# Kernel tuning notes

Measured on AMD Instinct MI355X. Metric: run time of the kernel, lower is better.

Reference implementation:

```python
import jax, jax.numpy as jnp
import numpy as np

B, T, C = 4, 2048, 1024
H, Dh = 16, 64
EPS = 1e-5

def _layernorm(x, g, b):
    mu = jnp.mean(x, axis=-1, keepdims=True)
    var = jnp.mean(jnp.square(x - mu), axis=-1, keepdims=True)
    return (x - mu) * jax.lax.rsqrt(var + EPS) * g + b

def setup_inputs() -> dict:
    key = jax.random.key(0)
    ks = jax.random.split(key, 12)
    s = lambda fan_in: 1.0 / np.sqrt(fan_in)
    return {
        "x":  jax.random.normal(ks[0], (B, T, C), dtype=jnp.float32),
        "Wq": jax.random.uniform(ks[1], (C, H * Dh), jnp.float32, -s(C), s(C)),
        "Wk": jax.random.uniform(ks[2], (C, H * Dh), jnp.float32, -s(C), s(C)),
        "Wv": jax.random.uniform(ks[3], (C, H * Dh), jnp.float32, -s(C), s(C)),
        "Wo": jax.random.uniform(ks[4], (H * Dh, C), jnp.float32, -s(H * Dh), s(H * Dh)),
        "bo": jnp.zeros((C,), jnp.float32),
        "W1": jax.random.uniform(ks[5], (C, 4 * C), jnp.float32, -s(C), s(C)),
        "b1": jnp.zeros((4 * C,), jnp.float32),
        "W2": jax.random.uniform(ks[6], (4 * C, C), jnp.float32, -s(4 * C), s(4 * C)),
        "b2": jnp.zeros((C,), jnp.float32),
        "g1": jnp.ones((C,), jnp.float32),
        "be1": jnp.zeros((C,), jnp.float32),
        "g2": jnp.ones((C,), jnp.float32),
        "be2": jnp.zeros((C,), jnp.float32),
    }

def reference(x, Wq, Wk, Wv, Wo, bo, W1, b1, W2, b2, g1, be1, g2, be2):
    # --- pre-LN attention ---
    h = _layernorm(x, g1, be1)                                   # [B,T,C]
    q = (h @ Wq).reshape(B, T, H, Dh)                            # per-head projections fused
    k = (h @ Wk).reshape(B, T, H, Dh)
    v = (h @ Wv).reshape(B, T, H, Dh)
    scores = jnp.einsum('bqhd,bkhd->bhqk', q, k) * (Dh ** -0.5)  # [B,H,T,T]
    causal = jnp.tril(jnp.ones((T, T), dtype=bool))
    scores = jnp.where(causal, scores, -jnp.inf)
    wei = jax.nn.softmax(scores, axis=-1)                        # dropout p=0 (eval)
    attn = jnp.einsum('bhqk,bkhd->bqhd', wei, v).reshape(B, T, H * Dh)
    x = x + attn @ Wo + bo
    # --- pre-LN MLP ---
    h2 = _layernorm(x, g2, be2)
    x = x + jax.nn.relu(h2 @ W1 + b1) @ W2 + b2
    return x
```

## Files before the change

### kernel.cpp

```cpp
#include <hip/hip_runtime.h>
#include <hip/hip_bf16.h>

typedef __hip_bfloat16 bf16;
typedef __attribute__((ext_vector_type(8))) short short8;
typedef __attribute__((ext_vector_type(4))) short s16x4;
typedef __attribute__((ext_vector_type(4))) float f32x4;

__device__ __forceinline__ float s2f(short s) {
    unsigned u = ((unsigned)(unsigned short)s) << 16;
    return __builtin_bit_cast(float, u);
}
__device__ __forceinline__ short f2s(float f) {
    bf16 h = __float2bfloat16(f);
    return __builtin_bit_cast(short, h);
}
__device__ __forceinline__ void gload_lds16(const void* g, void* l) {
    __builtin_amdgcn_global_load_lds(
        (const __attribute__((address_space(1))) unsigned int*)g,
        (__attribute__((address_space(3))) unsigned int*)l, 16, 0, 0);
}

#define PH_VM8  asm volatile("s_waitcnt vmcnt(8)" ::: "memory")
#define PH_VM4  asm volatile("s_waitcnt vmcnt(4)" ::: "memory")
#define PH_VM0  asm volatile("s_waitcnt vmcnt(0)" ::: "memory")
#define PH_BAR  __builtin_amdgcn_s_barrier()
#define PH_LGKM do { asm volatile("s_waitcnt lgkmcnt(0)" ::: "memory"); \
                     __builtin_amdgcn_sched_barrier(0); } while (0)

__global__ __launch_bounds__(256) void tconv_kernel(const float* __restrict__ src,
                                                    short* __restrict__ dst,
                                                    int R, int C) {
    __shared__ short tile[64][65];
    const int r0 = blockIdx.y * 64, c0 = blockIdx.x * 64;
    const int t = threadIdx.x;
    const int lr = t >> 2, lc = (t & 3) * 16;
    const float* sp = src + (size_t)(r0 + lr) * C + c0 + lc;
#pragma unroll
    for (int q = 0; q < 4; q++) {
        f32x4 v = *(const f32x4*)(const void*)(sp + q * 4);
#pragma unroll
        for (int j = 0; j < 4; j++) tile[lr][lc + q * 4 + j] = f2s(v[j]);
    }
    __syncthreads();
    short8 o0, o1;
#pragma unroll
    for (int j = 0; j < 8; j++) { o0[j] = tile[lc + j][lr]; o1[j] = tile[lc + 8 + j][lr]; }
    short* dp = dst + (size_t)(c0 + lr) * R + r0 + lc;
    *(short8*)(void*)dp = o0;
    *(short8*)(void*)(dp + 8) = o1;
}

__global__ __launch_bounds__(256) void ln_kernel(const float* __restrict__ x,
                                                 const float* __restrict__ g,
                                                 const float* __restrict__ beta,
                                                 bf16* __restrict__ out) {
    const int t = threadIdx.x;
    const int w = t >> 6, lane = t & 63;
    const int row = blockIdx.x * 4 + w;
    const float* xr = x + (size_t)row * 1024;
    float v[16];
    float s = 0.f, ss = 0.f;
#pragma unroll
    for (int p = 0; p < 4; p++) {
        f32x4 xv = *(const f32x4*)(const void*)(xr + p * 256 + lane * 4);
#pragma unroll
        for (int j = 0; j < 4; j++) {
            v[p * 4 + j] = xv[j];
            s += xv[j];
            ss += xv[j] * xv[j];
        }
    }
#pragma unroll
    for (int off = 32; off >= 1; off >>= 1) {
        s += __shfl_xor(s, off);
        ss += __shfl_xor(ss, off);
    }
    const float mu = s * (1.0f / 1024.0f);
    const float var = ss * (1.0f / 1024.0f) - mu * mu;
    const float rstd = rsqrtf(var + 1e-5f);
    short* orow = (short*)(void*)(out + (size_t)row * 1024);
#pragma unroll
    for (int p = 0; p < 4; p++) {
        const int c = p * 256 + lane * 4;
        f32x4 gv = *(const f32x4*)(const void*)(g + c);
        f32x4 bv = *(const f32x4*)(const void*)(beta + c);
        s16x4 o;
#pragma unroll
        for (int j = 0; j < 4; j++)
            o[j] = f2s((v[p * 4 + j] - mu) * rstd * gv[j] + bv[j]);
        *(s16x4*)(void*)(orow + c) = o;
    }
}

__global__ __launch_bounds__(256) void gemm64(const bf16* __restrict__ A,
                                              const bf16* __restrict__ Bt,
                                              const float* __restrict__ bias,
                                              const float* resid,
                                              void* Cp, int c_f32,
                                              int m_base, int N, int K,
                                              int relu_flag) {
    __shared__ short As[64 * 64];
    __shared__ short Bs[64 * 64];

    const int t = threadIdx.x;
    const int m0 = blockIdx.x * 64;
    const int n0 = blockIdx.y * 64;
    const int w = t >> 6;
    const int lane = t & 63;
    const int wm = (w >> 1) * 32;
    const int wn = (w & 1) * 32;

    const int sr = t >> 2, sk = (t & 3) * 8;
    const bf16* aA = A + (size_t)(m0 + sr) * K + sk;
    const bf16* aB = Bt + (size_t)(n0 + sr) * K + sk;
    short* ldsA0 = &As[w * 512];
    short* ldsA1 = &As[2048 + w * 512];
    short* ldsB0 = &Bs[w * 512];
    short* ldsB1 = &Bs[2048 + w * 512];

    const int l = lane & 15;
    const int lk = (lane >> 4) * 8;

    f32x4 acc[2][2] = {};

    for (int k0 = 0; k0 < K; k0 += 64) {
        __syncthreads();
        gload_lds16(aA + k0, ldsA0);
        gload_lds16(aA + k0 + 32, ldsA1);
        gload_lds16(aB + k0, ldsB0);
        gload_lds16(aB + k0 + 32, ldsB1);
        __syncthreads();
#pragma unroll
        for (int ks = 0; ks < 2; ks++) {
            short8 a0 = *(const short8*)&As[ks * 2048 + (wm + l) * 32 + lk];
            short8 a1 = *(const short8*)&As[ks * 2048 + (wm + 16 + l) * 32 + lk];
            short8 b0 = *(const short8*)&Bs[ks * 2048 + (wn + l) * 32 + lk];
            short8 b1 = *(const short8*)&Bs[ks * 2048 + (wn + 16 + l) * 32 + lk];
            acc[0][0] = __builtin_amdgcn_mfma_f32_16x16x32_bf16(a0, b0, acc[0][0], 0, 0, 0);
            acc[0][1] = __builtin_amdgcn_mfma_f32_16x16x32_bf16(a0, b1, acc[0][1], 0, 0, 0);
            acc[1][0] = __builtin_amdgcn_mfma_f32_16x16x32_bf16(a1, b0, acc[1][0], 0, 0, 0);
            acc[1][1] = __builtin_amdgcn_mfma_f32_16x16x32_bf16(a1, b1, acc[1][1], 0, 0, 0);
        }
    }

    const int lrow4 = (lane >> 4) * 4;
#pragma unroll
    for (int mi = 0; mi < 2; mi++)
#pragma unroll
        for (int r = 0; r < 4; r++) {
            const int grow = m_base + m0 + wm + mi * 16 + lrow4 + r;
#pragma unroll
            for (int ni = 0; ni < 2; ni++) {
                const int gcol = n0 + wn + ni * 16 + l;
                float val = acc[mi][ni][r];
                if (bias) val += bias[gcol];
                if (relu_flag) val = fmaxf(val, 0.f);
                const size_t ci = (size_t)grow * N + gcol;
                if (resid) val += resid[ci];
                if (c_f32) ((float*)Cp)[ci] = val;
                else        ((short*)Cp)[ci] = f2s(val);
            }
        }
}

#define MM_BLOCK(ACC)                                                        \
    do {                                                                     \
        __builtin_amdgcn_s_setprio(1);                                       \
        _Pragma("unroll")                                                    \
        for (int mi_ = 0; mi_ < 4; mi_++)                                    \
            _Pragma("unroll")                                                \
            for (int ni_ = 0; ni_ < 4; ni_++)                                \
                ACC[mi_][ni_] = __builtin_amdgcn_mfma_f32_16x16x32_bf16(     \
                    af[mi_], bf[ni_], ACC[mi_][ni_], 0, 0, 0);               \
        __builtin_amdgcn_s_setprio(0);                                       \
    } while (0)

__global__ __launch_bounds__(512, 2) void gemm256(const bf16* __restrict__ A,
                                                  const bf16* __restrict__ Bt,
                                                  const float* __restrict__ bias,
                                                  bf16* __restrict__ Cp,
                                                  int N, int relu_flag) {
    __shared__ char lds[131072];
    constexpr int NT = 16;

    const int t = threadIdx.x;
    const int w = t >> 6, lane = t & 63;
    const int l = lane & 15, g = lane >> 4;
    const int m0 = blockIdx.x * 256, n0 = blockIdx.y * 256;
    const int wm = (w >> 2) * 128, wn = (w & 3) * 64;
    const int qx = (g ^ ((l >> 1) & 3)) * 16;
    const int qh8 = (((lane & 3) ^ ((lane >> 3) & 3)) * 8);
    const int srow = w * 32 + (lane >> 2);
    const short* Asrc = (const short*)A;
    const short* Bsrc = (const short*)Bt;

    f32x4 accL[4][4] = {};
    f32x4 accH[4][4] = {};
    short8 af[4], bf[4];

    auto stage = [&](int th, int j) {
        const int ks = j >> 1, mat = j & 1;
        char* slot = lds + ((th & 1) << 16) + (mat << 15) + (ks << 14);
        const short* mp = mat ? Bsrc : Asrc;
        const int rowb = (mat ? n0 : m0);
        const int kc = th * 64 + ks * 32 + qh8;
        gload_lds16(mp + (size_t)(rowb + srow) * 1024 + kc,      slot + (w * 2) * 1024);
        gload_lds16(mp + (size_t)(rowb + srow + 16) * 1024 + kc, slot + (w * 2 + 1) * 1024);
    };
    auto lda = [&](const char* rb, int mi, int ks) -> short8 {
        return *(const short8*)(rb + (ks << 14) + (wm + mi * 16 + l) * 64 + qx);
    };
    auto ldb = [&](const char* rb, int ni, int ks) -> short8 {
        return *(const short8*)(rb + 32768 + (ks << 14) + (wn + ni * 16 + l) * 64 + qx);
    };

    stage(0, 0); stage(0, 1); stage(0, 2); stage(0, 3); stage(1, 0); stage(1, 1);

    for (int it = 0; it < NT - 1; ++it) {
        const char* rb = lds + ((it & 1) << 16);
        PH_VM8; PH_BAR;
#pragma unroll
        for (int i = 0; i < 4; i++) af[i] = lda(rb, i, 0);
#pragma unroll
        for (int i = 0; i < 4; i++) bf[i] = ldb(rb, i, 0);
        stage(it + 1, 2);
        PH_LGKM;
        MM_BLOCK(accL);
#pragma unroll
        for (int i = 0; i < 4; i++) af[i] = lda(rb, 4 + i, 0);
        stage(it + 1, 3);
        PH_BAR; PH_LGKM;
        MM_BLOCK(accH);
        PH_VM8; PH_BAR;
#pragma unroll
        for (int i = 0; i < 4; i++) af[i] = lda(rb, i, 1);
#pragma unroll
        for (int i = 0; i < 4; i++) bf[i] = ldb(rb, i, 1);
        if (it + 2 < NT) stage(it + 2, 0);
        PH_LGKM;
        MM_BLOCK(accL);
#pragma unroll
        for (int i = 0; i < 4; i++) af[i] = lda(rb, 4 + i, 1);
        if (it + 2 < NT) stage(it + 2, 1);
        PH_BAR; PH_LGKM;
        MM_BLOCK(accH);
    }
    {
        const char* rb = lds + (((NT - 1) & 1) << 16);
        PH_VM4; PH_BAR;
#pragma unroll
        for (int i = 0; i < 4; i++) af[i] = lda(rb, i, 0);
#pragma unroll
        for (int i = 0; i < 4; i++) bf[i] = ldb(rb, i, 0);
        PH_LGKM;
        MM_BLOCK(accL);
#pragma unroll
        for (int i = 0; i < 4; i++) af[i] = lda(rb, 4 + i, 0);
        PH_BAR; PH_LGKM;
        MM_BLOCK(accH);
        PH_VM0; PH_BAR;
#pragma unroll
        for (int i = 0; i < 4; i++) af[i] = lda(rb, i, 1);
#pragma unroll
        for (int i = 0; i < 4; i++) bf[i] = ldb(rb, i, 1);
        PH_LGKM;
        MM_BLOCK(accL);
#pragma unroll
        for (int i = 0; i < 4; i++) af[i] = lda(rb, 4 + i, 1);
        PH_BAR; PH_LGKM;
        MM_BLOCK(accH);
    }

#pragma unroll
    for (int half = 0; half < 2; half++)
#pragma unroll
        for (int mi = 0; mi < 4; mi++)
#pragma unroll
            for (int r = 0; r < 4; r++) {
                const int grow = m0 + wm + (half * 4 + mi) * 16 + g * 4 + r;
                short* crow = (short*)(void*)Cp + (size_t)grow * N;
#pragma unroll
                for (int ni = 0; ni < 4; ni++) {
                    const int gcol = n0 + wn + ni * 16 + l;
                    float val = half ? accH[mi][ni][r] : accL[mi][ni][r];
                    if (bias) val += bias[gcol];
                    if (relu_flag) val = fmaxf(val, 0.f);
                    crow[gcol] = f2s(val);
                }
            }
}

__global__ __launch_bounds__(256) void attn_kernel(const bf16* __restrict__ qkv,
                                                   bf16* __restrict__ o) {
    __shared__ short KsF[2][4096];
    __shared__ short Vt[64][72];
    __shared__ short Pl[4][32][76];

    const int bh = blockIdx.x;
    const int b = bh >> 4, h = bh & 15;
    const int qt = 15 - blockIdx.y;
    const int q0 = qt * 128;
    const size_t rbase = (size_t)b * 2048;
    const int hcol = h * 64;

    const int t = threadIdx.x;
    const int w = t >> 6;
    const int lane = t & 63;
    const int l = lane & 15;
    const int g = lane >> 4;
    const int sp = t >> 3;
    const int sb = (t & 7) * 8;

    const int qw0 = q0 + 32 * w;
    short8 qf[2][2];
#pragma unroll
    for (int mi = 0; mi < 2; mi++)
#pragma unroll
        for (int ks = 0; ks < 2; ks++) {
            const short* qp = (const short*)qkv +
                (rbase + qw0 + mi * 16 + l) * 3072 + hcol + ks * 32 + g * 8;
            short8 tv = *(const short8*)(const void*)qp;
            short8 sv;
#pragma unroll
            for (int e = 0; e < 8; e++) sv[e] = f2s(s2f(tv[e]) * 0.125f);
            qf[mi][ks] = sv;
        }

    const int key_a = w * 16 + (lane >> 3);
    const int kd = (lane & 7) ^ ((lane >> 3) & 7);
    const short* kgA = (const short*)qkv + (rbase + key_a) * 3072 + 1024 + hcol + kd * 8;
    const short* kgB = kgA + 8 * 3072;

    f32x4 o_acc[2][4] = {};
    f32x4 l_acc[2] = {};
    short8 onesf;
    {
        const short ov = (l == 0) ? (short)0x3F80 : (short)0;
#pragma unroll
        for (int e = 0; e < 8; e++) onesf[e] = ov;
    }
    const f32x4 s_init = {-12.f, -12.f, -12.f, -12.f};

    const int kt_max = (q0 + 127) >> 6;

    gload_lds16(kgA, &KsF[0][w * 1024]);
    gload_lds16(kgB, &KsF[0][w * 1024 + 512]);

    for (int kt = 0; kt <= kt_max; kt++) {
        const int k0 = kt * 64;
        const short* vg = (const short*)qkv + (rbase + k0 + 2 * sp) * 3072 + 2048 + hcol + sb;
        short8 vv0 = *(const short8*)(const void*)vg;
        short8 vv1 = *(const short8*)(const void*)(vg + 3072);
        PH_BAR;
        {
            const int kp = (kt < kt_max) ? (kt + 1) : kt;
            const size_t kof = (size_t)kp * 64 * 3072;
            gload_lds16(kgA + kof, &KsF[(kt + 1) & 1][w * 1024]);
            gload_lds16(kgB + kof, &KsF[(kt + 1) & 1][w * 1024 + 512]);
        }
        asm volatile("s_waitcnt vmcnt(2)" ::: "memory");
        __builtin_amdgcn_sched_barrier(0);
        {
            const int key = 2 * sp;
            const int cbk = key >> 3;
            const int kin = key & 7;
#pragma unroll
            for (int j = 0; j < 8; j++) {
                const int d = sb + j;
                const int col = ((cbk ^ (d >> 3)) << 3) + kin;
                int pk = (int)(unsigned short)vv0[j] | ((int)(unsigned short)vv1[j] << 16);
                *(int*)(void*)&Vt[d][col] = pk;
            }
        }
        asm volatile("s_waitcnt lgkmcnt(0)" ::: "memory");
        __builtin_amdgcn_sched_barrier(0);
        PH_BAR;

        if (k0 <= qw0 + 31) {
            const short* kb = &KsF[kt & 1][0];
            const bool needMask = (k0 + 63 > qw0);
            f32x4 s_acc[2][4];
#pragma unroll
            for (int mi = 0; mi < 2; mi++)
#pragma unroll
                for (int ni = 0; ni < 4; ni++) s_acc[mi][ni] = s_init;
#pragma unroll
            for (int ks = 0; ks < 2; ks++) {
                short8 kf[4];
#pragma unroll
                for (int ni = 0; ni < 4; ni++) {
                    const int key = ni * 16 + l;
                    const int c = key * 8 + ((ks * 4 + g) ^ (key & 7));
                    kf[ni] = *(const short8*)&kb[c * 8];
                }
#pragma unroll
                for (int mi = 0; mi < 2; mi++)
#pragma unroll
                    for (int ni = 0; ni < 4; ni++)
                        s_acc[mi][ni] = __builtin_amdgcn_mfma_f32_16x16x32_bf16(
                            qf[mi][ks], kf[ni], s_acc[mi][ni], 0, 0, 0);
            }
#pragma unroll
            for (int mi = 0; mi < 2; mi++)
#pragma unroll
                for (int r = 0; r < 4; r++) {
                    const int qg = qw0 + mi * 16 + 4 * g + r;
#pragma unroll
                    for (int ni = 0; ni < 4; ni++) {
                        float s = s_acc[mi][ni][r];
                        if (needMask && (k0 + ni * 16 + l > qg)) s = -1e30f;
                        Pl[w][mi * 16 + 4 * g + r][ni * 16 + l] = f2s(__expf(s));
                    }
                }
#pragma unroll
            for (int ks = 0; ks < 2; ks++) {
                short8 pf[2], vf[4];
#pragma unroll
                for (int mi = 0; mi < 2; mi++)
                    pf[mi] = *(const short8*)&Pl[w][mi * 16 + l][ks * 32 + g * 8];
#pragma unroll
                for (int nd = 0; nd < 4; nd++) {
                    const int d = nd * 16 + l;
                    const int cb = ks * 4 + g;
                    vf[nd] = *(const short8*)&Vt[d][((cb ^ (d >> 3)) << 3)];
                }
#pragma unroll
                for (int mi = 0; mi < 2; mi++) {
                    l_acc[mi] = __builtin_amdgcn_mfma_f32_16x16x32_bf16(
                        pf[mi], onesf, l_acc[mi], 0, 0, 0);
#pragma unroll
                    for (int nd = 0; nd < 4; nd++)
                        o_acc[mi][nd] = __builtin_amdgcn_mfma_f32_16x16x32_bf16(
                            pf[mi], vf[nd], o_acc[mi][nd], 0, 0, 0);
                }
            }
        }
    }

#pragma unroll
    for (int mi = 0; mi < 2; mi++)
#pragma unroll
        for (int r = 0; r < 4; r++) {
            float lsum = __shfl(l_acc[mi][r], lane & 48);
            const float inv = 1.0f / lsum;
            const int qg = qw0 + mi * 16 + 4 * g + r;
            short* op = (short*)(void*)(o + (rbase + qg) * 1024 + hcol);
#pragma unroll
            for (int nd = 0; nd < 4; nd++)
                op[nd * 16 + l] = f2s(o_acc[mi][nd][r] * inv);
        }
}

extern "C" void kernel_launch(void* const* d_in, const int* in_sizes, int n_in,
                              void* d_out, int out_size, void* d_ws, size_t ws_size,
                              hipStream_t stream) {
    const float* x   = (const float*)d_in[0];
    const float* Wq  = (const float*)d_in[1];
    const float* Wk  = (const float*)d_in[2];
    const float* Wv  = (const float*)d_in[3];
    const float* Wo  = (const float*)d_in[4];
    const float* bo  = (const float*)d_in[5];
    const float* W1  = (const float*)d_in[6];
    const float* b1  = (const float*)d_in[7];
    const float* W2  = (const float*)d_in[8];
    const float* b2  = (const float*)d_in[9];
    const float* g1  = (const float*)d_in[10];
    const float* be1 = (const float*)d_in[11];
    const float* g2  = (const float*)d_in[12];
    const float* be2 = (const float*)d_in[13];

    char* ws = (char*)d_ws;
    const size_t MB = (size_t)1024 * 1024;
    bf16*  s0  = (bf16*)(ws);
    bf16*  qkv = (bf16*)(ws + 16 * MB);
    short* WoT = (short*)(ws + 16 * MB);
    short* W1T = (short*)(ws);
    short* W2T = (short*)(ws + 8 * MB);
    bf16*  h2  = (bf16*)(ws + 16 * MB);
    bf16*  m1  = (bf16*)(ws + 32 * MB);
    short* WT  = (short*)d_out;
    float* x1  = (float*)d_out;

    const int M = 8192, C = 1024, F = 4096, MH = 4096;

    tconv_kernel<<<dim3(16, 16), 256, 0, stream>>>(Wq, WT,                   C, C);
    tconv_kernel<<<dim3(16, 16), 256, 0, stream>>>(Wk, WT + 1024 * 1024,     C, C);
    tconv_kernel<<<dim3(16, 16), 256, 0, stream>>>(Wv, WT + 2 * 1024 * 1024, C, C);

    ln_kernel<<<M / 4, 256, 0, stream>>>(x, g1, be1, s0);

    gemm256<<<dim3(M / 256, 3072 / 256), 512, 0, stream>>>(
        s0, (const bf16*)WT, nullptr, qkv, 3072, 0);

    attn_kernel<<<dim3(64, 16), 256, 0, stream>>>(qkv, s0);

    tconv_kernel<<<dim3(16, 16), 256, 0, stream>>>(Wo, WoT, C, C);
    gemm64<<<dim3(M / 64, C / 64), 256, 0, stream>>>(
        s0, (const bf16*)WoT, bo, x, x1, 1, 0, C, C, 0);

    tconv_kernel<<<dim3(64, 16), 256, 0, stream>>>(W1, W1T, C, F);
    tconv_kernel<<<dim3(16, 64), 256, 0, stream>>>(W2, W2T, F, C);

    ln_kernel<<<M / 4, 256, 0, stream>>>(x1, g2, be2, h2);

    for (int half = 0; half < 2; half++) {
        const bf16* Ah = h2 + (size_t)half * MH * C;
        gemm256<<<dim3(MH / 256, F / 256), 512, 0, stream>>>(
            Ah, (const bf16*)W1T, b1, m1, F, 1);
        gemm64<<<dim3(MH / 64, C / 64), 256, 0, stream>>>(
            m1, (const bf16*)W2T, b2, x1, d_out, 1, half * MH, C, F, 0);
    }
}
```

Baseline: 562.0 us.

## Transpose score MFMA for vectorized P stores, compute row sums in registers; swizzle GEMM blocks

The attention kernel swaps the MFMA operands so each lane holds four consecutive keys of one query row. The P tile can then be written to LDS with one 4-element vector store instead of scalar stores. The softmax denominator becomes a per-lane register sum finished with cross-lane shuffles, which removes the extra ones-vector MFMA per step. Separately, the GEMM remaps block indices with an 8-way swizzle to change the order tiles are scheduled, probably for L2 or cross-chip cache locality. This adds a few shuffles and index arithmetic, and the P store layout now depends on the transposed accumulator mapping.

```diff
diff --git a/kernel.cpp b/kernel.cpp
--- a/kernel.cpp
+++ b/kernel.cpp
@@ -186,7 +186,13 @@
     const int t = threadIdx.x;
     const int w = t >> 6, lane = t & 63;
     const int l = lane & 15, g = lane >> 4;
-    const int m0 = blockIdx.x * 256, n0 = blockIdx.y * 256;
+
+    const int nwg = gridDim.x * gridDim.y;
+    const int orig = blockIdx.y * gridDim.x + blockIdx.x;
+    const int swz = (orig & 7) * (nwg >> 3) + (orig >> 3);
+    const int m0 = (swz % gridDim.x) * 256;
+    const int n0 = (swz / gridDim.x) * 256;
+
     const int wm = (w >> 2) * 128, wn = (w & 3) * 64;
     const int qx = (g ^ ((l >> 1) & 3)) * 16;
     const int qh8 = (((lane & 3) ^ ((lane >> 3) & 3)) * 8);
@@ -332,13 +338,7 @@
     const short* kgB = kgA + 8 * 3072;
 
     f32x4 o_acc[2][4] = {};
-    f32x4 l_acc[2] = {};
-    short8 onesf;
-    {
-        const short ov = (l == 0) ? (short)0x3F80 : (short)0;
-#pragma unroll
-        for (int e = 0; e < 8; e++) onesf[e] = ov;
-    }
+    float l_sum[2] = {0.f, 0.f};
     const f32x4 s_init = {-12.f, -12.f, -12.f, -12.f};
 
     const int kt_max = (q0 + 127) >> 6;
@@ -398,20 +398,26 @@
 #pragma unroll
                     for (int ni = 0; ni < 4; ni++)
                         s_acc[mi][ni] = __builtin_amdgcn_mfma_f32_16x16x32_bf16(
-                            qf[mi][ks], kf[ni], s_acc[mi][ni], 0, 0, 0);
+                            kf[ni], qf[mi][ks], s_acc[mi][ni], 0, 0, 0);
             }
 #pragma unroll
-            for (int mi = 0; mi < 2; mi++)
-#pragma unroll
-                for (int r = 0; r < 4; r++) {
-                    const int qg = qw0 + mi * 16 + 4 * g + r;
-#pragma unroll
-                    for (int ni = 0; ni < 4; ni++) {
+            for (int mi = 0; mi < 2; mi++) {
+                const int qg = qw0 + mi * 16 + l;
+#pragma unroll
+                for (int ni = 0; ni < 4; ni++) {
+                    const int keyb = k0 + ni * 16 + 4 * g;
+                    s16x4 pv;
+#pragma unroll
+                    for (int r = 0; r < 4; r++) {
                         float s = s_acc[mi][ni][r];
-                        if (needMask && (k0 + ni * 16 + l > qg)) s = -1e30f;
-                        Pl[w][mi * 16 + 4 * g + r][ni * 16 + l] = f2s(__expf(s));
+                        if (needMask && (keyb + r > qg)) s = -1e30f;
+                        const float pe = __expf(s);
+                        l_sum[mi] += pe;
+                        pv[r] = f2s(pe);
                     }
+                    *(s16x4*)(void*)&Pl[w][mi * 16 + l][ni * 16 + 4 * g] = pv;
                 }
+            }
 #pragma unroll
             for (int ks = 0; ks < 2; ks++) {
                 short8 pf[2], vf[4];
@@ -425,23 +431,26 @@
                     vf[nd] = *(const short8*)&Vt[d][((cb ^ (d >> 3)) << 3)];
                 }
 #pragma unroll
-                for (int mi = 0; mi < 2; mi++) {
-                    l_acc[mi] = __builtin_amdgcn_mfma_f32_16x16x32_bf16(
-                        pf[mi], onesf, l_acc[mi], 0, 0, 0);
+                for (int mi = 0; mi < 2; mi++)
 #pragma unroll
                     for (int nd = 0; nd < 4; nd++)
                         o_acc[mi][nd] = __builtin_amdgcn_mfma_f32_16x16x32_bf16(
                             pf[mi], vf[nd], o_acc[mi][nd], 0, 0, 0);
-                }
             }
         }
     }
 
 #pragma unroll
+    for (int mi = 0; mi < 2; mi++) {
+        l_sum[mi] += __shfl_xor(l_sum[mi], 16);
+        l_sum[mi] += __shfl_xor(l_sum[mi], 32);
+    }
+
+#pragma unroll
     for (int mi = 0; mi < 2; mi++)
 #pragma unroll
         for (int r = 0; r < 4; r++) {
-            float lsum = __shfl(l_acc[mi][r], lane & 48);
+            const float lsum = __shfl(l_sum[mi], 4 * g + r);
             const float inv = 1.0f / lsum;
             const int qg = qw0 + mi * 16 + 4 * g + r;
             short* op = (short*)(void*)(o + (rbase + qg) * 1024 + hcol);
```

Measured after the change: 557.0 us. About the same (-0.9%).
